# Optimization experiments

Hardware: AMD Instinct MI355X
Metric: run time of the kernel (lower is better)

The kernel has to match this reference:

```python
import jax, jax.numpy as jnp
import numpy as np

B, S, UNITS = 32, 2048, 512

def setup_inputs() -> dict:
    key = jax.random.key(0)
    ks = jax.random.split(key, 8)
    sc = 1.0 / np.sqrt(UNITS)
    return {
        "s_prev": jax.random.normal(ks[0], (B, UNITS), jnp.float32),
        "hidden_states": jax.random.normal(ks[1], (B, S, UNITS), jnp.float32),
        "W_kernel": jax.random.normal(ks[2], (UNITS, UNITS), jnp.float32) * sc,
        "W_bias": jnp.zeros((UNITS,), jnp.float32),
        "U_kernel": jax.random.normal(ks[3], (UNITS, UNITS), jnp.float32) * sc,
        "U_bias": jnp.zeros((UNITS,), jnp.float32),
        "V_kernel": jax.random.normal(ks[4], (UNITS, 1), jnp.float32) * sc,
        "V_bias": jnp.zeros((1,), jnp.float32),
    }

def reference(s_prev, hidden_states, W_kernel, W_bias, U_kernel, U_bias, V_kernel, V_bias):
    # NOTE: faithful to the source code: U is applied to s_prev, W to hidden_states,
    # and the context is computed as softmax-weights * s_prev (as written, a quirk
    # of the original module), summed over the sequence axis.
    first = s_prev @ U_kernel + U_bias                      # (B, units)
    second = hidden_states @ W_kernel + W_bias              # (B, S, units)
    score = jnp.tanh(first[:, None, :] + second) @ V_kernel + V_bias  # (B, S, 1)
    weights = jax.nn.softmax(score, axis=1)                 # (B, S, 1)
    context = jnp.sum(weights * s_prev[:, None, :], axis=1) # (B, units)
    return context, weights
```

## Files before the change

### kernel.cpp

```cpp
#include <hip/hip_runtime.h>

#define NBATCH 32
#define SEQ    2048
#define NU     512

typedef __attribute__((ext_vector_type(8))) short bf16x8;
typedef __attribute__((ext_vector_type(4))) float f32x4;

__device__ __forceinline__ short bf16_rne(float f) {
  union { float f; unsigned u; } v; v.f = f;
  unsigned r = v.u + 0x7fffu + ((v.u >> 16) & 1u);
  return (short)(r >> 16);
}

__device__ __forceinline__ unsigned pk2(float lo, float hi) {
  return __builtin_amdgcn_perm(__float_as_uint(hi), __float_as_uint(lo), 0x07060302u);
}

__device__ __forceinline__ float fast_tanh(float x) {
  float ax = __builtin_fabsf(x);
  float t  = __expf(-2.0f * ax);
  float r  = (1.0f - t) / (1.0f + t);
  return x < 0.0f ? -r : r;
}

__global__ __launch_bounds__(256) void prep_all(const float* __restrict__ W,
                                                const float* __restrict__ sp,
                                                const float* __restrict__ U,
                                                const float* __restrict__ Ub,
                                                const float* __restrict__ Wb,
                                                short* __restrict__ WtSw,
                                                float* __restrict__ first) {
  __shared__ float srow[NU];
  if (blockIdx.x < 1024) {
    int idx = blockIdx.x * 256 + threadIdx.x;
    int C = idx >> 9, rem = idx & 511;
    int t = rem >> 6, up = (rem >> 3) & 7, e = rem & 7;
    int k = t * 64 + ((up ^ (C & 7)) << 3) + e;
    WtSw[idx] = bf16_rne(W[(size_t)k * NU + C]);
  } else {
    int blk = blockIdx.x - 1024;
    int b = blk >> 1, half = blk & 1, t = threadIdx.x;
    srow[t]       = sp[b * NU + t];
    srow[t + 256] = sp[b * NU + t + 256];
    __syncthreads();
    int col = half * 256 + t;
    float acc = Ub[col] + Wb[col];
    #pragma unroll 8
    for (int k = 0; k < NU; ++k) acc += srow[k] * U[(size_t)k * NU + col];
    first[b * NU + col] = acc;
  }
}

__global__ __launch_bounds__(512, 2) void attn8(
    const float* __restrict__ h,
    const short* __restrict__ WtSw,
    const float* __restrict__ first,
    const float* __restrict__ V,
    float* __restrict__ s0)
{
  __shared__ short Alds[2][256 * 64];
  __shared__ short Blds[2][256 * 64];

  const int tid  = threadIdx.x;
  const int lane = tid & 63;
  const int w    = tid >> 6;
  const int wr   = w >> 2, wc = w & 3;
  const int lr   = lane & 15, hi2 = lane >> 4;

  const int bid = blockIdx.x;
  const int lb  = (bid & 7) * 64 + (bid >> 3);
  const int panel = lb >> 1, half = lb & 1;
  const int rowbase = panel * 256;
  const int b = panel >> 3;

  const float* hstage = h + (size_t)(rowbase + (tid >> 2)) * NU + (tid & 3) * 16;
  const int rr = tid >> 2, u0 = (tid & 3) * 2;
  const int wby0 = rr * 128 + ((u0 ^ (rr & 7)) << 4);
  const int wby1 = rr * 128 + (((u0 | 1) ^ (rr & 7)) << 4);
  const short* wsrc = WtSw + (size_t)(half * 256 + w * 8 + (lane >> 3)) * NU + (lane & 7) * 8;

  int abase[8], bbase[4], s16[2];
  #pragma unroll
  for (int j = 0; j < 8; ++j) abase[j] = (wr * 128 + j * 16 + lr) * 128;
  #pragma unroll
  for (int j = 0; j < 4; ++j) bbase[j] = (wc * 64 + j * 16 + lr) * 128;
  #pragma unroll
  for (int ks = 0; ks < 2; ++ks) s16[ks] = ((ks * 4 + hi2) ^ (lr & 7)) << 4;

  f32x4 acc[8][4];
  #pragma unroll
  for (int mf = 0; mf < 8; ++mf)
    #pragma unroll
    for (int nf = 0; nf < 4; ++nf)
      acc[mf][nf] = (f32x4){0.f, 0.f, 0.f, 0.f};

  float4 ga0, ga1, ga2, ga3;

  #define STAGEB(nxt, t1, bh)                                                          \
    {                                                                                  \
      _Pragma("unroll")                                                                \
      for (int i = 0; i < 2; ++i)                                                      \
        __builtin_amdgcn_global_load_lds(                                              \
            (const __attribute__((address_space(1))) unsigned*)                        \
                (wsrc + (size_t)((bh) * 128 + i * 64) * NU + (t1) * 64),               \
            (__attribute__((address_space(3))) unsigned*)                              \
                (&Blds[nxt][(bh) * 8192 + i * 4096 + w * 512]), 16, 0, 0);             \
    }

  #define ISSA(t1, ah)                                                                 \
    {                                                                                  \
      const float* p = hstage + (size_t)(ah) * 128 * NU + (t1) * 64;                   \
      ga0 = *reinterpret_cast<const float4*>(p + 0);                                   \
      ga1 = *reinterpret_cast<const float4*>(p + 4);                                   \
      ga2 = *reinterpret_cast<const float4*>(p + 8);                                   \
      ga3 = *reinterpret_cast<const float4*>(p + 12);                                  \
    }

  #define CVTW(nxt, ah)                                                                \
    {                                                                                  \
      char* base = reinterpret_cast<char*>(&Alds[nxt][0]) + (ah) * 16384;              \
      uint4 ua, ub;                                                                    \
      ua.x = pk2(ga0.x, ga0.y); ua.y = pk2(ga0.z, ga0.w);                              \
      ua.z = pk2(ga1.x, ga1.y); ua.w = pk2(ga1.z, ga1.w);                              \
      ub.x = pk2(ga2.x, ga2.y); ub.y = pk2(ga2.z, ga2.w);                              \
      ub.z = pk2(ga3.x, ga3.y); ub.w = pk2(ga3.z, ga3.w);                              \
      *reinterpret_cast<uint4*>(base + wby0) = ua;                                     \
      *reinterpret_cast<uint4*>(base + wby1) = ub;                                     \
    }

  #define READ_A(mh, cur)                                                              \
    _Pragma("unroll")                                                                  \
    for (int mi = 0; mi < 4; ++mi)                                                     \
      _Pragma("unroll")                                                                \
      for (int ks = 0; ks < 2; ++ks)                                                   \
        af[mi][ks] = *reinterpret_cast<const bf16x8*>(                                 \
            reinterpret_cast<const char*>(&Alds[cur][0]) + abase[(mh) * 4 + mi] + s16[ks]);

  #define READ_BQ(BQ, nh, cur)                                                         \
    _Pragma("unroll")                                                                  \
    for (int ni = 0; ni < 2; ++ni)                                                     \
      _Pragma("unroll")                                                                \
      for (int ks = 0; ks < 2; ++ks)                                                   \
        BQ[ni][ks] = *reinterpret_cast<const bf16x8*>(                                 \
            reinterpret_cast<const char*>(&Blds[cur][0]) + bbase[(nh) * 2 + ni] + s16[ks]);

  #define MFMAQ(mh, nh, BQ)                                                            \
    __builtin_amdgcn_s_setprio(1);                                                     \
    _Pragma("unroll")                                                                  \
    for (int ks = 0; ks < 2; ++ks)                                                     \
      _Pragma("unroll")                                                                \
      for (int mi = 0; mi < 4; ++mi)                                                   \
        _Pragma("unroll")                                                              \
        for (int ni = 0; ni < 2; ++ni)                                                 \
          acc[(mh) * 4 + mi][(nh) * 2 + ni] = __builtin_amdgcn_mfma_f32_16x16x32_bf16( \
              af[mi][ks], BQ[ni][ks], acc[(mh) * 4 + mi][(nh) * 2 + ni], 0, 0, 0);     \
    __builtin_amdgcn_s_setprio(0);

  #define BAR                                                                          \
    asm volatile("" ::: "memory");                                                     \
    __builtin_amdgcn_s_barrier();                                                      \
    asm volatile("" ::: "memory");

  ISSA(0, 0);
  STAGEB(0, 0, 0); STAGEB(0, 0, 1);
  CVTW(0, 0);
  ISSA(0, 1);
  CVTW(0, 1);
  asm volatile("s_waitcnt vmcnt(0) lgkmcnt(0)" ::: "memory");
  __builtin_amdgcn_s_barrier();
  asm volatile("" ::: "memory");

  #pragma unroll 1
  for (int t = 0; t < 7; ++t) {
    const int cur = t & 1, nxt = cur ^ 1;
    bf16x8 af[4][2], bq0[2][2], bq1[2][2];
    READ_A(0, cur); READ_BQ(bq0, 0, cur);
    ISSA(t + 1, 0);
    STAGEB(nxt, t + 1, 0);
    BAR; MFMAQ(0, 0, bq0); BAR;
    READ_BQ(bq1, 1, cur);
    CVTW(nxt, 0);
    BAR; MFMAQ(0, 1, bq1); BAR;
    READ_A(1, cur);
    ISSA(t + 1, 1);
    STAGEB(nxt, t + 1, 1);
    BAR; MFMAQ(1, 0, bq0); BAR;
    CVTW(nxt, 1);
    BAR; MFMAQ(1, 1, bq1);
    asm volatile("s_waitcnt vmcnt(0) lgkmcnt(0)" ::: "memory");
    BAR;
  }

  {
    bf16x8 af[4][2], bq0[2][2], bq1[2][2];
    READ_A(0, 1); READ_BQ(bq0, 0, 1);
    BAR; MFMAQ(0, 0, bq0); BAR;
    READ_BQ(bq1, 1, 1);
    BAR; MFMAQ(0, 1, bq1); BAR;
    READ_A(1, 1);
    BAR; MFMAQ(1, 0, bq0); BAR;
    BAR; MFMAQ(1, 1, bq1);
  }

  #undef STAGEB
  #undef ISSA
  #undef CVTW
  #undef READ_A
  #undef READ_BQ
  #undef MFMAQ
  #undef BAR

  float fv[4], vv[4];
  #pragma unroll
  for (int nf = 0; nf < 4; ++nf) {
    int col = half * 256 + wc * 64 + nf * 16 + lr;
    fv[nf] = first[b * NU + col];
    vv[nf] = V[col];
  }
  #pragma unroll
  for (int mf = 0; mf < 8; ++mf) {
    f32x4 p;
    #pragma unroll
    for (int r = 0; r < 4; ++r) {
      float s = 0.f;
      #pragma unroll
      for (int nf = 0; nf < 4; ++nf)
        s += vv[nf] * fast_tanh(fv[nf] + acc[mf][nf][r]);
      p[r] = s;
    }
    #pragma unroll
    for (int m = 1; m < 16; m <<= 1) {
      #pragma unroll
      for (int r = 0; r < 4; ++r) p[r] += __shfl_xor(p[r], m, 64);
    }
    if (lr == 0) {
      const int rbase = rowbase + wr * 128 + mf * 16 + hi2 * 4;
      #pragma unroll
      for (int r = 0; r < 4; ++r) atomicAdd(&s0[rbase + r], p[r]);
    }
  }
}

__global__ __launch_bounds__(256) void softmax_ctx(const float* __restrict__ sp,
                                                   float* __restrict__ out) {
  const int b = blockIdx.x;
  const int t = threadIdx.x;
  float* wgt = out + NBATCH * NU + (size_t)b * SEQ;
  __shared__ float red[4];

  float v[8];
  float mx = -1e30f;
  #pragma unroll
  for (int i = 0; i < 8; ++i) { v[i] = wgt[t + i * 256]; mx = fmaxf(mx, v[i]); }
  #pragma unroll
  for (int m = 1; m < 64; m <<= 1) mx = fmaxf(mx, __shfl_xor(mx, m, 64));
  if ((t & 63) == 0) red[t >> 6] = mx;
  __syncthreads();
  mx = fmaxf(fmaxf(red[0], red[1]), fmaxf(red[2], red[3]));
  __syncthreads();

  float se = 0.f;
  #pragma unroll
  for (int i = 0; i < 8; ++i) { v[i] = __expf(v[i] - mx); se += v[i]; }
  #pragma unroll
  for (int m = 1; m < 64; m <<= 1) se += __shfl_xor(se, m, 64);
  if ((t & 63) == 0) red[t >> 6] = se;
  __syncthreads();
  se = red[0] + red[1] + red[2] + red[3];
  __syncthreads();

  const float inv = 1.0f / se;
  float sw = 0.f;
  #pragma unroll
  for (int i = 0; i < 8; ++i) { float wi = v[i] * inv; wgt[t + i * 256] = wi; sw += wi; }
  #pragma unroll
  for (int m = 1; m < 64; m <<= 1) sw += __shfl_xor(sw, m, 64);
  if ((t & 63) == 0) red[t >> 6] = sw;
  __syncthreads();
  sw = red[0] + red[1] + red[2] + red[3];

  out[b * NU + t]       = sp[b * NU + t] * sw;
  out[b * NU + t + 256] = sp[b * NU + t + 256] * sw;
}

extern "C" void kernel_launch(void* const* d_in, const int* in_sizes, int n_in,
                              void* d_out, int out_size, void* d_ws, size_t ws_size,
                              hipStream_t stream) {
  (void)in_sizes; (void)n_in; (void)out_size; (void)ws_size;
  const float* s_prev = (const float*)d_in[0];
  const float* h      = (const float*)d_in[1];
  const float* Wk     = (const float*)d_in[2];
  const float* Wb     = (const float*)d_in[3];
  const float* Uk     = (const float*)d_in[4];
  const float* Ub     = (const float*)d_in[5];
  const float* Vk     = (const float*)d_in[6];

  float* out   = (float*)d_out;
  float* first = (float*)d_ws;
  short* WtSw  = (short*)((char*)d_ws + 65536);
  float* s0    = out + NBATCH * NU;

  hipMemsetAsync(s0, 0, (size_t)NBATCH * SEQ * sizeof(float), stream);
  prep_all   <<<1088, 256, 0, stream>>>(Wk, s_prev, Uk, Ub, Wb, WtSw, first);
  attn8      <<< 512, 512, 0, stream>>>(h, WtSw, first, Vk, s0);
  softmax_ctx<<<  32, 256, 0, stream>>>(s_prev, out);
}
```

Baseline: 106.1 us.

## Shrink attention GEMM tile to 128x128 with 256-thread blocks and 2048 blocks

Reduces the per-block output tile from 256x256 to 128x128 and uses 4 waves of 256 threads instead of 8 waves of 512. The grid grows from 512 to 2048 blocks, and the staging of hidden states and W is redistributed. This gives more blocks per CU and better load balance and latency hiding. In exchange, each hidden-state row is now loaded and converted four times instead of twice, since there are 4 column quarters per row panel, and reuse within each tile is lower.

```diff
diff --git a/kernel.cpp b/kernel.cpp
--- a/kernel.cpp
+++ b/kernel.cpp
@@ -52,90 +52,107 @@
   }
 }
 
-__global__ __launch_bounds__(512, 2) void attn8(
+__global__ __launch_bounds__(256, 2) void attn8(
     const float* __restrict__ h,
     const short* __restrict__ WtSw,
     const float* __restrict__ first,
     const float* __restrict__ V,
     float* __restrict__ s0)
 {
-  __shared__ short Alds[2][256 * 64];
-  __shared__ short Blds[2][256 * 64];
+  __shared__ short Alds[2][128 * 64];
+  __shared__ short Blds[2][128 * 64];
 
   const int tid  = threadIdx.x;
   const int lane = tid & 63;
   const int w    = tid >> 6;
-  const int wr   = w >> 2, wc = w & 3;
+  const int wr   = w >> 1, wc = w & 1;
   const int lr   = lane & 15, hi2 = lane >> 4;
 
   const int bid = blockIdx.x;
-  const int lb  = (bid & 7) * 64 + (bid >> 3);
-  const int panel = lb >> 1, half = lb & 1;
-  const int rowbase = panel * 256;
-  const int b = panel >> 3;
-
-  const float* hstage = h + (size_t)(rowbase + (tid >> 2)) * NU + (tid & 3) * 16;
-  const int rr = tid >> 2, u0 = (tid & 3) * 2;
-  const int wby0 = rr * 128 + ((u0 ^ (rr & 7)) << 4);
-  const int wby1 = rr * 128 + (((u0 | 1) ^ (rr & 7)) << 4);
-  const short* wsrc = WtSw + (size_t)(half * 256 + w * 8 + (lane >> 3)) * NU + (lane & 7) * 8;
-
-  int abase[8], bbase[4], s16[2];
-  #pragma unroll
-  for (int j = 0; j < 8; ++j) abase[j] = (wr * 128 + j * 16 + lr) * 128;
+  const int lb  = (bid & 7) * 256 + (bid >> 3);
+  const int panel = lb >> 2, q = lb & 3;
+  const int rowbase = panel * 128;
+  const int b = panel >> 4;
+
+  const int rr = tid >> 1, uh = tid & 1;
+  const float* hstage = h + (size_t)(rowbase + rr) * NU + uh * 32;
+  int wby[4];
+  #pragma unroll
+  for (int i = 0; i < 4; ++i) {
+    int u = uh * 4 + i;
+    wby[i] = rr * 128 + ((u ^ (rr & 7)) << 4);
+  }
+
+  const short* wsrc = WtSw + (size_t)(q * 128 + w * 32 + (lane >> 3)) * NU + (lane & 7) * 8;
+
+  #define STAGEB(nxt, t1, i2)                                                          \
+    {                                                                                  \
+      _Pragma("unroll")                                                                \
+      for (int i = (i2) * 2; i < (i2) * 2 + 2; ++i)                                    \
+        __builtin_amdgcn_global_load_lds(                                              \
+            (const __attribute__((address_space(1))) unsigned*)                        \
+                (wsrc + (size_t)i * 8 * NU + (t1) * 64),                               \
+            (__attribute__((address_space(3))) unsigned*)                              \
+                (&Blds[nxt][(w * 32 + i * 8) * 64]), 16, 0, 0);                        \
+    }
+
+  int abase[4], bbase[4], s16[2];
+  #pragma unroll
+  for (int j = 0; j < 4; ++j) abase[j] = (wr * 64 + j * 16 + lr) * 128;
   #pragma unroll
   for (int j = 0; j < 4; ++j) bbase[j] = (wc * 64 + j * 16 + lr) * 128;
   #pragma unroll
   for (int ks = 0; ks < 2; ++ks) s16[ks] = ((ks * 4 + hi2) ^ (lr & 7)) << 4;
 
-  f32x4 acc[8][4];
-  #pragma unroll
-  for (int mf = 0; mf < 8; ++mf)
+  f32x4 acc[4][4];
+  #pragma unroll
+  for (int mf = 0; mf < 4; ++mf)
     #pragma unroll
     for (int nf = 0; nf < 4; ++nf)
       acc[mf][nf] = (f32x4){0.f, 0.f, 0.f, 0.f};
 
   float4 ga0, ga1, ga2, ga3;
-
-  #define STAGEB(nxt, t1, bh)                                                          \
-    {                                                                                  \
-      _Pragma("unroll")                                                                \
-      for (int i = 0; i < 2; ++i)                                                      \
-        __builtin_amdgcn_global_load_lds(                                              \
-            (const __attribute__((address_space(1))) unsigned*)                        \
-                (wsrc + (size_t)((bh) * 128 + i * 64) * NU + (t1) * 64),               \
-            (__attribute__((address_space(3))) unsigned*)                              \
-                (&Blds[nxt][(bh) * 8192 + i * 4096 + w * 512]), 16, 0, 0);             \
-    }
-
-  #define ISSA(t1, ah)                                                                 \
-    {                                                                                  \
-      const float* p = hstage + (size_t)(ah) * 128 * NU + (t1) * 64;                   \
+  float4 gb0, gb1, gb2, gb3;
+
+  #define ISSA0(t1)                                                                    \
+    { const float* p = hstage + (t1) * 64;                                             \
       ga0 = *reinterpret_cast<const float4*>(p + 0);                                   \
       ga1 = *reinterpret_cast<const float4*>(p + 4);                                   \
       ga2 = *reinterpret_cast<const float4*>(p + 8);                                   \
-      ga3 = *reinterpret_cast<const float4*>(p + 12);                                  \
-    }
-
-  #define CVTW(nxt, ah)                                                                \
-    {                                                                                  \
-      char* base = reinterpret_cast<char*>(&Alds[nxt][0]) + (ah) * 16384;              \
-      uint4 ua, ub;                                                                    \
+      ga3 = *reinterpret_cast<const float4*>(p + 12); }
+  #define ISSA1(t1)                                                                    \
+    { const float* p = hstage + (t1) * 64 + 16;                                        \
+      gb0 = *reinterpret_cast<const float4*>(p + 0);                                   \
+      gb1 = *reinterpret_cast<const float4*>(p + 4);                                   \
+      gb2 = *reinterpret_cast<const float4*>(p + 8);                                   \
+      gb3 = *reinterpret_cast<const float4*>(p + 12); }
+
+  #define CVTW0(nxt)                                                                   \
+    { char* base = reinterpret_cast<char*>(&Alds[nxt][0]);                             \
+      uint4 ua;                                                                        \
       ua.x = pk2(ga0.x, ga0.y); ua.y = pk2(ga0.z, ga0.w);                              \
       ua.z = pk2(ga1.x, ga1.y); ua.w = pk2(ga1.z, ga1.w);                              \
-      ub.x = pk2(ga2.x, ga2.y); ub.y = pk2(ga2.z, ga2.w);                              \
-      ub.z = pk2(ga3.x, ga3.y); ub.w = pk2(ga3.z, ga3.w);                              \
-      *reinterpret_cast<uint4*>(base + wby0) = ua;                                     \
-      *reinterpret_cast<uint4*>(base + wby1) = ub;                                     \
-    }
+      *reinterpret_cast<uint4*>(base + wby[0]) = ua;                                   \
+      ua.x = pk2(ga2.x, ga2.y); ua.y = pk2(ga2.z, ga2.w);                              \
+      ua.z = pk2(ga3.x, ga3.y); ua.w = pk2(ga3.z, ga3.w);                              \
+      *reinterpret_cast<uint4*>(base + wby[1]) = ua; }
+  #define CVTW1(nxt)                                                                   \
+    { char* base = reinterpret_cast<char*>(&Alds[nxt][0]);                             \
+      uint4 ua;                                                                        \
+      ua.x = pk2(gb0.x, gb0.y); ua.y = pk2(gb0.z, gb0.w);                              \
+      ua.z = pk2(gb1.x, gb1.y); ua.w = pk2(gb1.z, gb1.w);                              \
+      *reinterpret_cast<uint4*>(base + wby[2]) = ua;                                   \
+      ua.x = pk2(gb2.x, gb2.y); ua.y = pk2(gb2.z, gb2.w);                              \
+      ua.z = pk2(gb3.x, gb3.y); ua.w = pk2(gb3.z, gb3.w);                              \
+      *reinterpret_cast<uint4*>(base + wby[3]) = ua; }
 
   #define READ_A(mh, cur)                                                              \
     _Pragma("unroll")                                                                  \
-    for (int mi = 0; mi < 4; ++mi)                                                     \
+    for (int mi = 0; mi < 2; ++mi)                                                     \
       _Pragma("unroll")                                                                \
       for (int ks = 0; ks < 2; ++ks)                                                   \
         af[mi][ks] = *reinterpret_cast<const bf16x8*>(                                 \
-            reinterpret_cast<const char*>(&Alds[cur][0]) + abase[(mh) * 4 + mi] + s16[ks]);
+            reinterpret_cast<const char*>(&Alds[cur][0]) + abase[(mh) * 2 + mi] + s16[ks]);
 
   #define READ_BQ(BQ, nh, cur)                                                         \
     _Pragma("unroll")                                                                  \
@@ -150,11 +167,11 @@
     _Pragma("unroll")                                                                  \
     for (int ks = 0; ks < 2; ++ks)                                                     \
       _Pragma("unroll")                                                                \
-      for (int mi = 0; mi < 4; ++mi)                                                   \
+      for (int mi = 0; mi < 2; ++mi)                                                   \
         _Pragma("unroll")                                                              \
         for (int ni = 0; ni < 2; ++ni)                                                 \
-          acc[(mh) * 4 + mi][(nh) * 2 + ni] = __builtin_amdgcn_mfma_f32_16x16x32_bf16( \
-              af[mi][ks], BQ[ni][ks], acc[(mh) * 4 + mi][(nh) * 2 + ni], 0, 0, 0);     \
+          acc[(mh) * 2 + mi][(nh) * 2 + ni] = __builtin_amdgcn_mfma_f32_16x16x32_bf16( \
+              af[mi][ks], BQ[ni][ks], acc[(mh) * 2 + mi][(nh) * 2 + ni], 0, 0, 0);     \
     __builtin_amdgcn_s_setprio(0);
 
   #define BAR                                                                          \
@@ -162,11 +179,9 @@
     __builtin_amdgcn_s_barrier();                                                      \
     asm volatile("" ::: "memory");
 
-  ISSA(0, 0);
+  ISSA0(0); ISSA1(0);
   STAGEB(0, 0, 0); STAGEB(0, 0, 1);
-  CVTW(0, 0);
-  ISSA(0, 1);
-  CVTW(0, 1);
+  CVTW0(0); CVTW1(0);
   asm volatile("s_waitcnt vmcnt(0) lgkmcnt(0)" ::: "memory");
   __builtin_amdgcn_s_barrier();
   asm volatile("" ::: "memory");
@@ -174,26 +189,26 @@
   #pragma unroll 1
   for (int t = 0; t < 7; ++t) {
     const int cur = t & 1, nxt = cur ^ 1;
-    bf16x8 af[4][2], bq0[2][2], bq1[2][2];
+    bf16x8 af[2][2], bq0[2][2], bq1[2][2];
     READ_A(0, cur); READ_BQ(bq0, 0, cur);
-    ISSA(t + 1, 0);
+    ISSA0(t + 1);
     STAGEB(nxt, t + 1, 0);
     BAR; MFMAQ(0, 0, bq0); BAR;
     READ_BQ(bq1, 1, cur);
-    CVTW(nxt, 0);
+    ISSA1(t + 1);
+    STAGEB(nxt, t + 1, 1);
     BAR; MFMAQ(0, 1, bq1); BAR;
     READ_A(1, cur);
-    ISSA(t + 1, 1);
-    STAGEB(nxt, t + 1, 1);
+    CVTW0(nxt);
     BAR; MFMAQ(1, 0, bq0); BAR;
-    CVTW(nxt, 1);
+    CVTW1(nxt);
     BAR; MFMAQ(1, 1, bq1);
     asm volatile("s_waitcnt vmcnt(0) lgkmcnt(0)" ::: "memory");
     BAR;
   }
 
   {
-    bf16x8 af[4][2], bq0[2][2], bq1[2][2];
+    bf16x8 af[2][2], bq0[2][2], bq1[2][2];
     READ_A(0, 1); READ_BQ(bq0, 0, 1);
     BAR; MFMAQ(0, 0, bq0); BAR;
     READ_BQ(bq1, 1, 1);
@@ -204,8 +219,10 @@
   }
 
   #undef STAGEB
-  #undef ISSA
-  #undef CVTW
+  #undef ISSA0
+  #undef ISSA1
+  #undef CVTW0
+  #undef CVTW1
   #undef READ_A
   #undef READ_BQ
   #undef MFMAQ
@@ -214,12 +231,12 @@
   float fv[4], vv[4];
   #pragma unroll
   for (int nf = 0; nf < 4; ++nf) {
-    int col = half * 256 + wc * 64 + nf * 16 + lr;
+    int col = q * 128 + wc * 64 + nf * 16 + lr;
     fv[nf] = first[b * NU + col];
     vv[nf] = V[col];
   }
   #pragma unroll
-  for (int mf = 0; mf < 8; ++mf) {
+  for (int mf = 0; mf < 4; ++mf) {
     f32x4 p;
     #pragma unroll
     for (int r = 0; r < 4; ++r) {
@@ -235,7 +252,7 @@
       for (int r = 0; r < 4; ++r) p[r] += __shfl_xor(p[r], m, 64);
     }
     if (lr == 0) {
-      const int rbase = rowbase + wr * 128 + mf * 16 + hi2 * 4;
+      const int rbase = rowbase + wr * 64 + mf * 16 + hi2 * 4;
       #pragma unroll
       for (int r = 0; r < 4; ++r) atomicAdd(&s0[rbase + r], p[r]);
     }
@@ -303,6 +320,6 @@
 
   hipMemsetAsync(s0, 0, (size_t)NBATCH * SEQ * sizeof(float), stream);
   prep_all   <<<1088, 256, 0, stream>>>(Wk, s_prev, Uk, Ub, Wb, WtSw, first);
-  attn8      <<< 512, 512, 0, stream>>>(h, WtSw, first, Vk, s0);
+  attn8      <<<2048, 256, 0, stream>>>(h, WtSw, first, Vk, s0);
   softmax_ctx<<<  32, 256, 0, stream>>>(s_prev, out);
 }
```

Result: slower. 142.2 us (+33.9%).
